# Kernel optimization log

Hardware: AMD Instinct MI355X
Metric: run time of the kernel (lower is better)

The kernel has to match this reference:

```python
import jax, jax.numpy as jnp
import numpy as np

M, K, L, OUT = 16, 64, 6, 128
IN_CH = 2 + 1 + 1 + 1 + 4 * L  # 29
HID_IN = 128 * 2 + 4           # 260


def setup_inputs() -> dict:
    key = jax.random.key(0)
    ks = jax.random.split(key, 5)
    N = 2_000_000
    P = jax.random.normal(ks[0], (N, 2), jnp.float32) * 2.0
    def lin(k, i, o):
        return jax.random.normal(k, (i, o), jnp.float32) / np.float32(np.sqrt(i))
    return {
        'P': P,
        'W1': lin(ks[1], IN_CH, 64), 'b1': jnp.zeros((64,), jnp.float32),
        'W2': lin(ks[2], 64, 128),   'b2': jnp.zeros((128,), jnp.float32),
        'W3': lin(ks[3], HID_IN, 128), 'b3': jnp.zeros((128,), jnp.float32),
        'W4': lin(ks[4], 128, OUT),  'b4': jnp.zeros((OUT,), jnp.float32),
    }


def _fps(P, m):
    # furthest point sampling, seeded at index 0 (standard convention)
    N = P.shape[0]
    def step(carry, _):
        min_d, last_idx = carry
        last = P[last_idx]
        d = jnp.sum((P - last) ** 2, axis=-1)          # [N]
        min_d = jnp.minimum(min_d, d)
        nxt = jnp.argmax(min_d)
        return (min_d, nxt), last_idx
    init = (jnp.full((N,), jnp.finfo(jnp.float32).max, jnp.float32), jnp.int32(0))
    (_, _), idxs = jax.lax.scan(step, init, None, length=m)
    return idxs  # [m] int


def _gelu(x):
    return jax.nn.gelu(x, approximate=False)  # torch nn.GELU default = erf


def reference(P, W1, b1, W2, b2, W3, b3, W4, b4):
    c_idx = jax.lax.stop_gradient(_fps(P, M))
    C = P[c_idx]                                       # [M,2]
    # brute-force kNN: expanded squared distance avoids [M,N,2] intermediate
    Ps = jax.lax.stop_gradient(P)
    Cs = jax.lax.stop_gradient(C)
    d2 = (jnp.sum(Ps ** 2, -1)[None, :]
          - 2.0 * Cs @ Ps.T
          + jnp.sum(Cs ** 2, -1)[:, None])             # [M,N]
    _, nidx = jax.lax.top_k(-d2, K)                    # [M,K]
    patch = P[nidx]                                    # [M,K,2]
    delta = patch - C[:, None, :]                      # [M,K,2]
    r = jnp.linalg.norm(delta, axis=-1, keepdims=True) # [M,K,1]
    theta = jnp.arctan2(delta[..., 1:2], delta[..., 0:1])
    freqs = (2.0 ** jnp.arange(L)).astype(jnp.float32) # [L]
    ang = delta[..., None, :] * freqs[:, None]         # [M,K,L,2]
    ff = jnp.concatenate([jnp.sin(ang), jnp.cos(ang)], -1).reshape(M, K, 4 * L)
    per_pt = jnp.concatenate([delta, r, jnp.sin(theta), jnp.cos(theta), ff], -1)  # [M,K,29]
    h = _gelu(per_pt @ W1 + b1)
    h = _gelu(h @ W2 + b2)                             # [M,K,128]
    h_max = h.max(axis=1)
    h_mean = h.mean(axis=1)
    rr = r[..., 0]                                     # [M,K]
    stats = jnp.stack([rr.mean(1), rr.max(1), rr.min(1), rr.std(1, ddof=1)], -1)  # [M,4]
    z = jnp.concatenate([h_max, h_mean, stats], -1)    # [M,260]
    F = _gelu(z @ W3 + b3) @ W4 + b4                   # [M,OUT]
    return F, C
```

## Files before the change

### kernel.cpp

```cpp
#include <hip/hip_runtime.h>
#include <math.h>

#define MCENT 16
#define KNN   64
#define NBINS 512
#define RBINS 256
#define CAP   7936
#define FPSB  512
#define FPST  256
#define MLPT  1024

__device__ __forceinline__ float gelu_f(float x){
    return 0.5f * x * (1.0f + erff(x * 0.70710678118654752440f));
}

__global__ __launch_bounds__(FPST) void fps_step(
    const float* __restrict__ P, int N,
    float* __restrict__ min_d,
    unsigned long long* __restrict__ partials,
    int k,
    float* __restrict__ cxy,
    float* __restrict__ outC,
    unsigned int* __restrict__ ghist,
    unsigned int* __restrict__ cnt)
{
    const int lane = threadIdx.x & 63;
    const int wid  = threadIdx.x >> 6;
    __shared__ unsigned long long wred[FPST/64];
    __shared__ int s_cur;

    if (k == 0){
        int gi = blockIdx.x*FPST + threadIdx.x;
        if (gi < MCENT*NBINS) ghist[gi] = 0u;
        if (gi < MCENT) cnt[gi] = 0u;
    }

    int cur = 0;
    if (k > 0){
        unsigned long long pb = 0ULL;
        for (int i = threadIdx.x; i < FPSB; i += FPST){
            unsigned long long v = partials[(k-1)*FPSB + i];
            if (v > pb) pb = v;
        }
#pragma unroll
        for (int off = 32; off > 0; off >>= 1){
            unsigned long long o = __shfl_xor(pb, off, 64);
            if (o > pb) pb = o;
        }
        if (lane == 0) wred[wid] = pb;
        __syncthreads();
        if (threadIdx.x == 0){
            unsigned long long b = wred[0];
#pragma unroll
            for (int w = 1; w < FPST/64; ++w) if (wred[w] > b) b = wred[w];
            s_cur = (int)(0xFFFFFFFFu - (unsigned)(b & 0xFFFFFFFFu));
        }
        __syncthreads();
        cur = s_cur;
    }

    if (blockIdx.x == 0 && threadIdx.x == 0){
        float cx = P[2*cur], cy = P[2*cur+1];
        cxy[2*k] = cx; cxy[2*k+1] = cy;
        outC[2*k] = cx; outC[2*k+1] = cy;
    }
    if (k >= MCENT-1) return;

    const float cx = P[2*cur], cy = P[2*cur+1];
    unsigned long long bk = 0ULL;
    const int T  = gridDim.x * FPST;
    const int NP = N >> 1;
    for (int q = blockIdx.x*FPST + threadIdx.x; q < NP; q += T){
        float4 p = ((const float4*)P)[q];
        float dx0 = __fsub_rn(p.x, cx), dy0 = __fsub_rn(p.y, cy);
        float d0  = __fadd_rn(__fmul_rn(dx0,dx0), __fmul_rn(dy0,dy0));
        float dx1 = __fsub_rn(p.z, cx), dy1 = __fsub_rn(p.w, cy);
        float d1  = __fadd_rn(__fmul_rn(dx1,dx1), __fmul_rn(dy1,dy1));
        float2 mp;
        if (k == 0){ mp.x = d0; mp.y = d1; }
        else {
            mp = ((const float2*)min_d)[q];
            mp.x = fminf(mp.x, d0); mp.y = fminf(mp.y, d1);
        }
        ((float2*)min_d)[q] = mp;
        int g = 2*q;
        unsigned long long k0 =
            ((unsigned long long)__float_as_uint(mp.x) << 32)
            | (unsigned long long)(0xFFFFFFFFu - (unsigned)g);
        unsigned long long k1 =
            ((unsigned long long)__float_as_uint(mp.y) << 32)
            | (unsigned long long)(0xFFFFFFFFu - (unsigned)(g+1));
        if (k0 > bk) bk = k0;
        if (k1 > bk) bk = k1;
    }
    if ((N & 1) && blockIdx.x == 0 && threadIdx.x == 0){
        int g = N-1;
        float dx = __fsub_rn(P[2*g], cx), dy = __fsub_rn(P[2*g+1], cy);
        float d  = __fadd_rn(__fmul_rn(dx,dx), __fmul_rn(dy,dy));
        float nm = (k == 0) ? d : fminf(min_d[g], d);
        min_d[g] = nm;
        unsigned long long kk =
            ((unsigned long long)__float_as_uint(nm) << 32)
            | (unsigned long long)(0xFFFFFFFFu - (unsigned)g);
        if (kk > bk) bk = kk;
    }
#pragma unroll
    for (int off = 32; off > 0; off >>= 1){
        unsigned long long o = __shfl_xor(bk, off, 64);
        if (o > bk) bk = o;
    }
    if (lane == 0) wred[wid] = bk;
    __syncthreads();
    if (threadIdx.x == 0){
        unsigned long long b = wred[0];
#pragma unroll
        for (int w = 1; w < FPST/64; ++w) if (wred[w] > b) b = wred[w];
        partials[k*FPSB + blockIdx.x] = b;
    }
}

__global__ __launch_bounds__(256) void hist_kernel(
    const float* __restrict__ P, int N,
    const float* __restrict__ cxy,
    unsigned int* __restrict__ ghist,
    unsigned int* __restrict__ rhist)
{
    __shared__ unsigned int h[MCENT*NBINS];
    __shared__ float scx[MCENT], scy[MCENT], scs2[MCENT];
    {
        int gi = blockIdx.x*blockDim.x + threadIdx.x;
        if (gi < MCENT*RBINS) rhist[gi] = 0u;
    }
    for (int i = threadIdx.x; i < MCENT*NBINS; i += blockDim.x) h[i] = 0u;
    if (threadIdx.x < MCENT){
        float a = cxy[2*threadIdx.x], b = cxy[2*threadIdx.x+1];
        scx[threadIdx.x] = a; scy[threadIdx.x] = b;
        scs2[threadIdx.x] = __fadd_rn(__fmul_rn(a,a), __fmul_rn(b,b));
    }
    __syncthreads();
    const int T    = gridDim.x * blockDim.x;
    const int NP16 = (N >> 1) >> 4;
    for (int q = blockIdx.x*blockDim.x + threadIdx.x; q < NP16; q += T){
        float4 p = ((const float4*)P)[(size_t)q << 4];
        float ps20 = __fadd_rn(__fmul_rn(p.x,p.x), __fmul_rn(p.y,p.y));
        float ps21 = __fadd_rn(__fmul_rn(p.z,p.z), __fmul_rn(p.w,p.w));
#pragma unroll
        for (int m = 0; m < MCENT; ++m){
            float dot0 = __fadd_rn(__fmul_rn(scx[m],p.x), __fmul_rn(scy[m],p.y));
            float d20  = __fadd_rn(__fsub_rn(ps20, __fmul_rn(2.0f,dot0)), scs2[m]);
            atomicAdd(&h[m*NBINS + (__float_as_uint(fmaxf(d20,0.0f)) >> 22)], 1u);
            float dot1 = __fadd_rn(__fmul_rn(scx[m],p.z), __fmul_rn(scy[m],p.w));
            float d21  = __fadd_rn(__fsub_rn(ps21, __fmul_rn(2.0f,dot1)), scs2[m]);
            atomicAdd(&h[m*NBINS + (__float_as_uint(fmaxf(d21,0.0f)) >> 22)], 1u);
        }
    }
    __syncthreads();
    for (int i = threadIdx.x; i < MCENT*NBINS; i += blockDim.x){
        unsigned v = h[i];
        if (v) atomicAdd(&ghist[i], v);
    }
}

__global__ void thr_kernel(const unsigned int* __restrict__ ghist,
                           float* __restrict__ thr,
                           float* __restrict__ sc2){
    int m = threadIdx.x;
    if (m < MCENT){
        unsigned cum = 0; int B = NBINS-1;
        for (int b = 0; b < NBINS; ++b){
            cum += ghist[m*NBINS + b];
            if (cum >= KNN){ B = b; break; }
        }
        float t = __uint_as_float((unsigned)(B+1) << 22);
        thr[m] = t;
        sc2[m] = 255.0f / t;
    }
}

__global__ __launch_bounds__(256) void refine_kernel(
    const float* __restrict__ P, int N,
    const float* __restrict__ cxy,
    const float* __restrict__ sc2,
    unsigned int* __restrict__ rhist)
{
    __shared__ unsigned int h[MCENT*RBINS];
    __shared__ float scx[MCENT], scy[MCENT], scs2[MCENT], ssc[MCENT];
    for (int i = threadIdx.x; i < MCENT*RBINS; i += blockDim.x) h[i] = 0u;
    if (threadIdx.x < MCENT){
        float a = cxy[2*threadIdx.x], b = cxy[2*threadIdx.x+1];
        scx[threadIdx.x]=a; scy[threadIdx.x]=b;
        scs2[threadIdx.x]=__fadd_rn(__fmul_rn(a,a),__fmul_rn(b,b));
        ssc[threadIdx.x]=sc2[threadIdx.x];
    }
    __syncthreads();
    const int T  = gridDim.x * blockDim.x;
    const int NP = N >> 1;
    for (int q = blockIdx.x*blockDim.x + threadIdx.x; q < NP; q += T){
        float4 p = ((const float4*)P)[q];
        float ps20 = __fadd_rn(__fmul_rn(p.x,p.x), __fmul_rn(p.y,p.y));
        float ps21 = __fadd_rn(__fmul_rn(p.z,p.z), __fmul_rn(p.w,p.w));
#pragma unroll
        for (int m = 0; m < MCENT; ++m){
            float dot0 = __fadd_rn(__fmul_rn(scx[m],p.x), __fmul_rn(scy[m],p.y));
            float d20  = __fadd_rn(__fsub_rn(ps20, __fmul_rn(2.0f,dot0)), scs2[m]);
            int b0 = (int)(fmaxf(d20, 0.0f) * ssc[m]);
            if (b0 < RBINS) atomicAdd(&h[m*RBINS + b0], 1u);
            float dot1 = __fadd_rn(__fmul_rn(scx[m],p.z), __fmul_rn(scy[m],p.w));
            float d21  = __fadd_rn(__fsub_rn(ps21, __fmul_rn(2.0f,dot1)), scs2[m]);
            int b1 = (int)(fmaxf(d21, 0.0f) * ssc[m]);
            if (b1 < RBINS) atomicAdd(&h[m*RBINS + b1], 1u);
        }
    }
    if ((N & 1) && blockIdx.x == 0 && threadIdx.x == 0){
        int g = N-1;
        float x = P[2*g], y = P[2*g+1];
        float ps2 = __fadd_rn(__fmul_rn(x,x), __fmul_rn(y,y));
        for (int m = 0; m < MCENT; ++m){
            float dot = __fadd_rn(__fmul_rn(scx[m],x), __fmul_rn(scy[m],y));
            float d2  = __fadd_rn(__fsub_rn(ps2, __fmul_rn(2.0f,dot)), scs2[m]);
            int b = (int)(fmaxf(d2, 0.0f) * ssc[m]);
            if (b < RBINS) atomicAdd(&h[m*RBINS + b], 1u);
        }
    }
    __syncthreads();
    for (int i = threadIdx.x; i < MCENT*RBINS; i += blockDim.x){
        unsigned v = h[i];
        if (v) atomicAdd(&rhist[i], v);
    }
}

__global__ void thr2_kernel(const unsigned int* __restrict__ rhist,
                            int* __restrict__ B2){
    int m = threadIdx.x;
    if (m < MCENT){
        unsigned cum = 0; int B = RBINS-1;
        for (int b = 0; b < RBINS; ++b){
            cum += rhist[m*RBINS + b];
            if (cum >= KNN){ B = b; break; }
        }
        B2[m] = B;
    }
}

__global__ __launch_bounds__(256) void collect_kernel(
    const float* __restrict__ P, int N,
    const float* __restrict__ cxy,
    const float* __restrict__ sc2,
    const int* __restrict__ B2,
    unsigned int* __restrict__ cnt,
    float* __restrict__ cd2,
    int* __restrict__ cidx)
{
    __shared__ float scx[MCENT], scy[MCENT], scs2[MCENT], ssc[MCENT];
    __shared__ int sB2[MCENT];
    if (threadIdx.x < MCENT){
        float a = cxy[2*threadIdx.x], b = cxy[2*threadIdx.x+1];
        scx[threadIdx.x]=a; scy[threadIdx.x]=b;
        scs2[threadIdx.x]=__fadd_rn(__fmul_rn(a,a),__fmul_rn(b,b));
        ssc[threadIdx.x]=sc2[threadIdx.x];
        sB2[threadIdx.x]=B2[threadIdx.x];
    }
    __syncthreads();
    const int T  = gridDim.x*blockDim.x;
    const int NP = N >> 1;
    for (int q = blockIdx.x*blockDim.x + threadIdx.x; q < NP; q += T){
        float4 p = ((const float4*)P)[q];
        float ps20 = __fadd_rn(__fmul_rn(p.x,p.x), __fmul_rn(p.y,p.y));
        float ps21 = __fadd_rn(__fmul_rn(p.z,p.z), __fmul_rn(p.w,p.w));
        int g = 2*q;
#pragma unroll
        for (int m = 0; m < MCENT; ++m){
            float dot0 = __fadd_rn(__fmul_rn(scx[m],p.x), __fmul_rn(scy[m],p.y));
            float d20  = __fadd_rn(__fsub_rn(ps20, __fmul_rn(2.0f,dot0)), scs2[m]);
            if ((int)(fmaxf(d20,0.0f) * ssc[m]) <= sB2[m]){
                unsigned pos = atomicAdd(&cnt[m], 1u);
                if (pos < CAP){ cd2[m*CAP+pos]=d20; cidx[m*CAP+pos]=g; }
            }
            float dot1 = __fadd_rn(__fmul_rn(scx[m],p.z), __fmul_rn(scy[m],p.w));
            float d21  = __fadd_rn(__fsub_rn(ps21, __fmul_rn(2.0f,dot1)), scs2[m]);
            if ((int)(fmaxf(d21,0.0f) * ssc[m]) <= sB2[m]){
                unsigned pos = atomicAdd(&cnt[m], 1u);
                if (pos < CAP){ cd2[m*CAP+pos]=d21; cidx[m*CAP+pos]=g+1; }
            }
        }
    }
    if ((N & 1) && blockIdx.x == 0 && threadIdx.x == 0){
        int g = N-1;
        float x = P[2*g], y = P[2*g+1];
        float ps2 = __fadd_rn(__fmul_rn(x,x), __fmul_rn(y,y));
        for (int m = 0; m < MCENT; ++m){
            float dot = __fadd_rn(__fmul_rn(scx[m],x), __fmul_rn(scy[m],y));
            float d2  = __fadd_rn(__fsub_rn(ps2, __fmul_rn(2.0f,dot)), scs2[m]);
            if ((int)(fmaxf(d2,0.0f) * ssc[m]) <= sB2[m]){
                unsigned pos = atomicAdd(&cnt[m], 1u);
                if (pos < CAP){ cd2[m*CAP+pos]=d2; cidx[m*CAP+pos]=g; }
            }
        }
    }
}

__global__ __launch_bounds__(256) void select_kernel(
    const unsigned int* __restrict__ cnt,
    const float* __restrict__ cd2,
    const int* __restrict__ cidx,
    int* __restrict__ nbr)
{
    const int m = blockIdx.x;
    __shared__ unsigned long long keys[CAP];
    unsigned c = cnt[m]; if (c > CAP) c = CAP;
    for (int i = threadIdx.x; i < (int)c; i += 256){
        unsigned u = __float_as_uint(cd2[m*CAP+i]);
        u = (u & 0x80000000u) ? ~u : (u | 0x80000000u);
        keys[i] = ((unsigned long long)u << 32)
                | (unsigned long long)(unsigned)cidx[m*CAP+i];
    }
    __syncthreads();
    for (int i = threadIdx.x; i < (int)c; i += 256){
        unsigned long long ki = keys[i];
        int rank = 0;
        for (int j = 0; j < (int)c; ++j) rank += (keys[j] < ki);
        if (rank < KNN) nbr[m*KNN + rank] = (int)(unsigned)(ki & 0xFFFFFFFFu);
    }
}

__global__ __launch_bounds__(MLPT) void mlp_kernel(
    const float* __restrict__ P,
    const float* __restrict__ cxy,
    const int* __restrict__ nbr,
    const float* __restrict__ W1, const float* __restrict__ b1,
    const float* __restrict__ W2, const float* __restrict__ b2,
    const float* __restrict__ W3, const float* __restrict__ b3,
    const float* __restrict__ W4, const float* __restrict__ b4,
    float* __restrict__ outF)
{
    const int m = blockIdx.x;
    const int tid = threadIdx.x;
    __shared__ float feat[KNN][32];
    __shared__ float h1s[KNN][64];
    __shared__ float sW1[29*64];
    __shared__ float sW2[64*128];
    __shared__ float pmax[8][128], psum[8][128];
    __shared__ float z[260];
    __shared__ float part[8][128];
    __shared__ float zz[128];

    {
        const float4* s2 = (const float4*)W2;
        float4* d2 = (float4*)sW2;
        d2[tid]        = s2[tid];
        d2[tid + 1024] = s2[tid + 1024];
        if (tid < 464) ((float4*)sW1)[tid] = ((const float4*)W1)[tid];
    }

    const float cx = cxy[2*m], cy = cxy[2*m+1];
    if (tid < KNN){
        int g = nbr[m*KNN + tid];
        float dx = P[2*g]   - cx;
        float dy = P[2*g+1] - cy;
        float r  = sqrtf(dx*dx + dy*dy);
        float th = atan2f(dy, dx);
        feat[tid][0]=dx; feat[tid][1]=dy; feat[tid][2]=r;
        feat[tid][3]=sinf(th); feat[tid][4]=cosf(th);
        float fx = dx, fy = dy;
#pragma unroll
        for (int l = 0; l < 6; ++l){
            feat[tid][5+4*l+0]=sinf(fx);
            feat[tid][5+4*l+1]=sinf(fy);
            feat[tid][5+4*l+2]=cosf(fx);
            feat[tid][5+4*l+3]=cosf(fy);
            fx += fx; fy += fy;
        }
    }
    __syncthreads();

#pragma unroll
    for (int rep = 0; rep < 4; ++rep){
        int o = rep*MLPT + tid;
        int k = o >> 6, j = o & 63;
        float acc = b1[j];
#pragma unroll
        for (int c = 0; c < 29; ++c) acc += feat[k][c] * sW1[c*64 + j];
        h1s[k][j] = gelu_f(acc);
    }
    __syncthreads();

    {
        int j = tid & 127, kh = tid >> 7;
        float lmax = -3.402823466e+38f, lsum = 0.f;
        for (int kk = 0; kk < 8; ++kk){
            int k = kh*8 + kk;
            float acc = b2[j];
#pragma unroll 8
            for (int i = 0; i < 64; ++i) acc += h1s[k][i] * sW2[i*128 + j];
            float v = gelu_f(acc);
            lmax = fmaxf(lmax, v);
            lsum += v;
        }
        pmax[kh][j] = lmax; psum[kh][j] = lsum;
    }
    __syncthreads();
    if (tid < 128){
        float mx = pmax[0][tid], sm = psum[0][tid];
#pragma unroll
        for (int w = 1; w < 8; ++w){ mx = fmaxf(mx, pmax[w][tid]); sm += psum[w][tid]; }
        z[tid]       = mx;
        z[128 + tid] = sm * (1.0f/64.0f);
    }
    if (tid >= 128 && tid < 192){
        int l = tid - 128;
        float r = feat[l][2];
        float s = r, mx = r, mn = r;
        for (int off = 1; off < 64; off <<= 1){
            s  += __shfl_xor(s, off, 64);
            mx  = fmaxf(mx, __shfl_xor(mx, off, 64));
            mn  = fminf(mn, __shfl_xor(mn, off, 64));
        }
        float mean = s * (1.0f/64.0f);
        float dv = (r-mean)*(r-mean);
        for (int off = 1; off < 64; off <<= 1) dv += __shfl_xor(dv, off, 64);
        if (l == 0){
            z[256]=mean; z[257]=mx; z[258]=mn; z[259]=sqrtf(dv*(1.0f/63.0f));
        }
    }
    __syncthreads();

    {
        int j = tid & 127, seg = tid >> 7;
        int i0  = (seg < 4) ? seg*33 : 132 + (seg-4)*32;
        int cntn = (seg < 4) ? 33 : 32;
        float acc = 0.f;
        for (int i = i0; i < i0 + cntn; ++i) acc += z[i]*W3[i*128+j];
        part[seg][j] = acc;
    }
    __syncthreads();
    if (tid < 128){
        float a = part[0][tid];
#pragma unroll
        for (int w = 1; w < 8; ++w) a += part[w][tid];
        zz[tid] = gelu_f(a + b3[tid]);
    }
    __syncthreads();
    {
        int j = tid & 127, seg = tid >> 7;
        float acc = 0.f;
#pragma unroll
        for (int i = seg*16; i < seg*16+16; ++i) acc += zz[i]*W4[i*128+j];
        part[seg][j] = acc;
    }
    __syncthreads();
    if (tid < 128){
        float a = part[0][tid];
#pragma unroll
        for (int w = 1; w < 8; ++w) a += part[w][tid];
        outF[m*128 + tid] = a + b4[tid];
    }
}

extern "C" void kernel_launch(void* const* d_in, const int* in_sizes, int n_in,
                              void* d_out, int out_size, void* d_ws, size_t ws_size,
                              hipStream_t stream)
{
    const float* P  = (const float*)d_in[0];
    const float* W1 = (const float*)d_in[1];
    const float* b1 = (const float*)d_in[2];
    const float* W2 = (const float*)d_in[3];
    const float* b2 = (const float*)d_in[4];
    const float* W3 = (const float*)d_in[5];
    const float* b3 = (const float*)d_in[6];
    const float* W4 = (const float*)d_in[7];
    const float* b4 = (const float*)d_in[8];
    int N = in_sizes[0] / 2;
    float* outF = (float*)d_out;
    float* outC = outF + MCENT*128;
    (void)n_in; (void)out_size; (void)ws_size;

    char* base = (char*)d_ws;
    size_t off = 0;
    auto take = [&](size_t bytes)->char*{
        char* p = base + off;
        off = (off + bytes + 255) & ~(size_t)255;
        return p;
    };
    unsigned long long* partials = (unsigned long long*)take((size_t)MCENT*FPSB*8);
    float* cxy         = (float*)take(MCENT*2*4);
    unsigned int* ghist= (unsigned int*)take(MCENT*NBINS*4);
    unsigned int* rhist= (unsigned int*)take(MCENT*RBINS*4);
    unsigned int* cnt  = (unsigned int*)take(MCENT*4);
    float* thr         = (float*)take(MCENT*4);
    float* sc2         = (float*)take(MCENT*4);
    int*   B2          = (int*)  take(MCENT*4);
    int*   nbr         = (int*)  take(MCENT*KNN*4);
    float* cd2         = (float*)take((size_t)MCENT*CAP*4);
    int*   cidx        = (int*)  take((size_t)MCENT*CAP*4);
    float* min_d       = (float*)take((size_t)N*4);

    for (int k = 0; k < MCENT-1; ++k)
        fps_step<<<FPSB, FPST, 0, stream>>>(P, N, min_d, partials, k, cxy, outC,
                                            ghist, cnt);
    fps_step<<<1, FPST, 0, stream>>>(P, N, min_d, partials, MCENT-1, cxy, outC,
                                     ghist, cnt);

    hist_kernel<<<128, 256, 0, stream>>>(P, N, cxy, ghist, rhist);
    thr_kernel<<<1, 64, 0, stream>>>(ghist, thr, sc2);
    refine_kernel<<<256, 256, 0, stream>>>(P, N, cxy, sc2, rhist);
    thr2_kernel<<<1, 64, 0, stream>>>(rhist, B2);
    collect_kernel<<<512, 256, 0, stream>>>(P, N, cxy, sc2, B2, cnt, cd2, cidx);
    select_kernel<<<MCENT, 256, 0, stream>>>(cnt, cd2, cidx, nbr);
    mlp_kernel<<<MCENT, MLPT, 0, stream>>>(P, cxy, nbr, W1,b1,W2,b2,W3,b3,W4,b4, outF);
}
```

Baseline: 312.5 us.

## Partition streaming kernels by XCD, double FPS grid, fold final FPS step into hist

Streaming loops in fps_step, refine and collect now give each of the 8 XCDs (picked by blockIdx & 7) a contiguous eighth of the point array, so each XCD's L2 sees a compact range. The FPS grid grows from 512 to 1024 blocks. The last single-block fps_step launch is removed, and hist_kernel now reduces the step-14 partials itself to find centroid 15, saving one launch. Each hist block repeats that reduction, and the XCD mapping relies on round-robin block dispatch across XCDs.

```diff
diff --git a/kernel.cpp b/kernel.cpp
--- a/kernel.cpp
+++ b/kernel.cpp
@@ -6,12 +6,21 @@
 #define NBINS 512
 #define RBINS 256
 #define CAP   7936
-#define FPSB  512
+#define FPSB  1024
 #define FPST  256
 #define MLPT  1024
 
 __device__ __forceinline__ float gelu_f(float x){
     return 0.5f * x * (1.0f + erff(x * 0.70710678118654752440f));
+}
+
+__device__ __forceinline__ void xcd_slice(int NP, int B, int bid, int tpb, int tid,
+                                          int* q0, int* s1, int* step){
+    int xcd = bid & 7, j = bid >> 3, Bx = B >> 3;
+    long long np = NP;
+    *q0   = (int)((np * xcd) >> 3) + j*tpb + tid;
+    *s1   = (int)((np * (xcd+1)) >> 3);
+    *step = Bx * tpb;
 }
 
 __global__ __launch_bounds__(FPST) void fps_step(
@@ -64,13 +73,13 @@
         cxy[2*k] = cx; cxy[2*k+1] = cy;
         outC[2*k] = cx; outC[2*k+1] = cy;
     }
-    if (k >= MCENT-1) return;
 
     const float cx = P[2*cur], cy = P[2*cur+1];
     unsigned long long bk = 0ULL;
-    const int T  = gridDim.x * FPST;
     const int NP = N >> 1;
-    for (int q = blockIdx.x*FPST + threadIdx.x; q < NP; q += T){
+    int q0, s1, st;
+    xcd_slice(NP, gridDim.x, blockIdx.x, FPST, threadIdx.x, &q0, &s1, &st);
+    for (int q = q0; q < s1; q += st){
         float4 p = ((const float4*)P)[q];
         float dx0 = __fsub_rn(p.x, cx), dy0 = __fsub_rn(p.y, cy);
         float d0  = __fadd_rn(__fmul_rn(dx0,dx0), __fmul_rn(dy0,dy0));
@@ -121,19 +130,54 @@
 
 __global__ __launch_bounds__(256) void hist_kernel(
     const float* __restrict__ P, int N,
-    const float* __restrict__ cxy,
+    const unsigned long long* __restrict__ partials,
+    float* __restrict__ cxy,
+    float* __restrict__ outC,
     unsigned int* __restrict__ ghist,
     unsigned int* __restrict__ rhist)
 {
     __shared__ unsigned int h[MCENT*NBINS];
     __shared__ float scx[MCENT], scy[MCENT], scs2[MCENT];
+    __shared__ unsigned long long wred[4];
+    __shared__ int s_cur;
+
+    {
+        unsigned long long pb = 0ULL;
+        for (int i = threadIdx.x; i < FPSB; i += 256){
+            unsigned long long v = partials[14*FPSB + i];
+            if (v > pb) pb = v;
+        }
+#pragma unroll
+        for (int off = 32; off > 0; off >>= 1){
+            unsigned long long o = __shfl_xor(pb, off, 64);
+            if (o > pb) pb = o;
+        }
+        if ((threadIdx.x & 63) == 0) wred[threadIdx.x >> 6] = pb;
+        __syncthreads();
+        if (threadIdx.x == 0){
+            unsigned long long b = wred[0];
+#pragma unroll
+            for (int w = 1; w < 4; ++w) if (wred[w] > b) b = wred[w];
+            s_cur = (int)(0xFFFFFFFFu - (unsigned)(b & 0xFFFFFFFFu));
+        }
+        __syncthreads();
+    }
+    const int cur15 = s_cur;
+    const float c15x = P[2*cur15], c15y = P[2*cur15+1];
+    if (blockIdx.x == 0 && threadIdx.x == 0){
+        cxy[30] = c15x; cxy[31] = c15y;
+        outC[30] = c15x; outC[31] = c15y;
+    }
+
     {
         int gi = blockIdx.x*blockDim.x + threadIdx.x;
         if (gi < MCENT*RBINS) rhist[gi] = 0u;
     }
     for (int i = threadIdx.x; i < MCENT*NBINS; i += blockDim.x) h[i] = 0u;
     if (threadIdx.x < MCENT){
-        float a = cxy[2*threadIdx.x], b = cxy[2*threadIdx.x+1];
+        float a, b;
+        if (threadIdx.x == 15){ a = c15x; b = c15y; }
+        else { a = cxy[2*threadIdx.x]; b = cxy[2*threadIdx.x+1]; }
         scx[threadIdx.x] = a; scy[threadIdx.x] = b;
         scs2[threadIdx.x] = __fadd_rn(__fmul_rn(a,a), __fmul_rn(b,b));
     }
@@ -193,9 +237,10 @@
         ssc[threadIdx.x]=sc2[threadIdx.x];
     }
     __syncthreads();
-    const int T  = gridDim.x * blockDim.x;
     const int NP = N >> 1;
-    for (int q = blockIdx.x*blockDim.x + threadIdx.x; q < NP; q += T){
+    int q0, s1, st;
+    xcd_slice(NP, gridDim.x, blockIdx.x, 256, threadIdx.x, &q0, &s1, &st);
+    for (int q = q0; q < s1; q += st){
         float4 p = ((const float4*)P)[q];
         float ps20 = __fadd_rn(__fmul_rn(p.x,p.x), __fmul_rn(p.y,p.y));
         float ps21 = __fadd_rn(__fmul_rn(p.z,p.z), __fmul_rn(p.w,p.w));
@@ -261,9 +306,10 @@
         sB2[threadIdx.x]=B2[threadIdx.x];
     }
     __syncthreads();
-    const int T  = gridDim.x*blockDim.x;
     const int NP = N >> 1;
-    for (int q = blockIdx.x*blockDim.x + threadIdx.x; q < NP; q += T){
+    int q0, s1, st;
+    xcd_slice(NP, gridDim.x, blockIdx.x, 256, threadIdx.x, &q0, &s1, &st);
+    for (int q = q0; q < s1; q += st){
         float4 p = ((const float4*)P)[q];
         float ps20 = __fadd_rn(__fmul_rn(p.x,p.x), __fmul_rn(p.y,p.y));
         float ps21 = __fadd_rn(__fmul_rn(p.z,p.z), __fmul_rn(p.w,p.w));
@@ -497,10 +543,8 @@
     for (int k = 0; k < MCENT-1; ++k)
         fps_step<<<FPSB, FPST, 0, stream>>>(P, N, min_d, partials, k, cxy, outC,
                                             ghist, cnt);
-    fps_step<<<1, FPST, 0, stream>>>(P, N, min_d, partials, MCENT-1, cxy, outC,
-                                     ghist, cnt);
-
-    hist_kernel<<<128, 256, 0, stream>>>(P, N, cxy, ghist, rhist);
+
+    hist_kernel<<<128, 256, 0, stream>>>(P, N, partials, cxy, outC, ghist, rhist);
     thr_kernel<<<1, 64, 0, stream>>>(ghist, thr, sc2);
     refine_kernel<<<256, 256, 0, stream>>>(P, N, cxy, sc2, rhist);
     thr2_kernel<<<1, 64, 0, stream>>>(rhist, B2);
```

New measurement: 310.4 us. Within noise of the previous version (-0.7%).
